# Kernel optimization log

Hardware: AMD Instinct MI355X
Metric: run time of the kernel (lower is better)

The kernel has to match this reference:

```python
import jax, jax.numpy as jnp
import numpy as np

# Model/config constants
N = 2048          # total nodes in batch
G = 32            # number of graphs
NPG = 64          # nodes per graph (N = G * NPG)
E = 16384         # total edges (E//G per graph, unique within graph)
HIDDEN = 256
N_HEADS = 8
HEAD_DIM = HIDDEN // N_HEADS
EDGE_FEAT = 16
SCALE = HEAD_DIM ** -0.5


def setup_inputs() -> dict:
    key = jax.random.key(0)
    ks = jax.random.split(key, 16)
    nodes = jax.random.normal(ks[0], (N, HIDDEN), dtype=jnp.float32)
    edges = jax.random.normal(ks[1], (E, EDGE_FEAT), dtype=jnp.float32)
    n_node = jnp.full((G,), NPG, dtype=jnp.int32)
    # Unique (sender, receiver) pairs within each graph block
    epg = E // G
    gkeys = jax.random.split(ks[2], G)
    perm = jax.vmap(lambda k: jax.random.permutation(k, NPG * NPG)[:epg])(gkeys)  # [G, epg]
    so = perm // NPG
    ro = perm % NPG
    base = (jnp.arange(G, dtype=jnp.int32) * NPG)[:, None]
    senders = (base + so).reshape(-1).astype(jnp.int32)
    receivers = (base + ro).reshape(-1).astype(jnp.int32)
    init = 0.02
    Wq = jax.random.normal(ks[3], (HIDDEN, HIDDEN), jnp.float32) * init
    Wk = jax.random.normal(ks[4], (HIDDEN, HIDDEN), jnp.float32) * init
    Wv = jax.random.normal(ks[5], (HIDDEN, HIDDEN), jnp.float32) * init
    Wo = jax.random.normal(ks[6], (HIDDEN, HIDDEN), jnp.float32) * init
    We = jax.random.normal(ks[7], (EDGE_FEAT, N_HEADS), jnp.float32) * init
    bq = jnp.zeros((HIDDEN,), jnp.float32)
    bk = jnp.zeros((HIDDEN,), jnp.float32)
    bv = jnp.zeros((HIDDEN,), jnp.float32)
    bo = jnp.zeros((HIDDEN,), jnp.float32)
    be = jnp.zeros((N_HEADS,), jnp.float32)
    return {"nodes": nodes, "edges": edges, "n_node": n_node,
            "senders": senders, "receivers": receivers,
            "Wq": Wq, "bq": bq, "Wk": Wk, "bk": bk, "Wv": Wv, "bv": bv,
            "Wo": Wo, "bo": bo, "We": We, "be": be}


def reference(nodes, edges, n_node, senders, receivers,
              Wq, bq, Wk, bk, Wv, bv, Wo, bo, We, be):
    n_nodes = nodes.shape[0]
    n_graphs = n_node.shape[0]
    q = (nodes @ Wq + bq).reshape(n_nodes, N_HEADS, HEAD_DIM)
    k = (nodes @ Wk + bk).reshape(n_nodes, N_HEADS, HEAD_DIM)
    v = (nodes @ Wv + bv).reshape(n_nodes, N_HEADS, HEAD_DIM)
    scores = jnp.einsum('ihd,jhd->ijh', q, k) * SCALE  # [N, N, H]
    graph_idx = jnp.repeat(jnp.arange(n_graphs), n_node, total_repeat_length=n_nodes)
    same_graph = graph_idx[:, None] == graph_idx[None, :]
    scores = scores + jnp.where(same_graph[:, :, None], 0.0, -1e9)
    # Edge bias scattered into [N, N, H] at (receiver, sender)
    edge_bias = edges @ We + be  # [E, H]
    edge_bias_matrix = jnp.zeros((n_nodes, n_nodes, N_HEADS), dtype=scores.dtype)
    edge_bias_matrix = edge_bias_matrix.at[receivers, senders].set(edge_bias)
    scores = scores + edge_bias_matrix
    attn = jax.nn.softmax(scores, axis=1)  # softmax over key axis j
    out = jnp.einsum('ijh,jhd->ihd', attn, v).reshape(n_nodes, HIDDEN)
    return out @ Wo + bo
```

## Files before the change

### kernel.cpp

```cpp
#include <hip/hip_runtime.h>

#define N_NODES 2048
#define N_GRAPHS 32
#define NPG 64
#define N_EDGES 16384
#define EPG 512
#define HIDDEN 256
#define NHEADS 8
#define HEADDIM 32
#define EDGEFEAT 16
#define ATT_SCALE 0.17677669529663687f

typedef unsigned short u16;
typedef __attribute__((ext_vector_type(8))) short bf16x8;
typedef __attribute__((ext_vector_type(4))) float f32x4;

__device__ __forceinline__ u16 f2b(float f) {
    unsigned x = __float_as_uint(f);
    return (u16)((x + 0x7fffu + ((x >> 16) & 1u)) >> 16);
}
__device__ __forceinline__ float b2f(u16 u) {
    return __uint_as_float(((unsigned)u) << 16);
}
__device__ __forceinline__ unsigned pack2(float a, float b) {
    return (unsigned)f2b(a) | ((unsigned)f2b(b) << 16);
}

__global__ __launch_bounds__(256)
void setup_pre(const float* __restrict__ nodes,
               const float* __restrict__ Wq, const float* __restrict__ Wk,
               const float* __restrict__ Wv, const float* __restrict__ Wo,
               const float* __restrict__ edges, const float* __restrict__ We,
               const float* __restrict__ be,
               const int* __restrict__ senders, const int* __restrict__ receivers,
               u16* __restrict__ nodesb,
               u16* __restrict__ WT,
               uint2* __restrict__ ebp,
               float* __restrict__ out)
{
    const int b = blockIdx.x, tid = threadIdx.x;
    __shared__ float sf[64 * 65];

    if (b < 64) {
        const int m = b >> 4, tile = b & 15;
        const int k0 = (tile >> 2) * 64, n0 = (tile & 3) * 64;
        const float* src = (m == 0) ? Wq : (m == 1) ? Wk : (m == 2) ? Wv : Wo;
        u16* dst = WT + m * 65536;
        #pragma unroll
        for (int i = 0; i < 4; ++i) {
            const int idx = i * 256 + tid, kr = idx >> 4, c4 = idx & 15;
            float4 x = *(const float4*)(src + (size_t)(k0 + kr) * HIDDEN + n0 + c4 * 4);
            sf[kr * 65 + c4 * 4 + 0] = x.x;
            sf[kr * 65 + c4 * 4 + 1] = x.y;
            sf[kr * 65 + c4 * 4 + 2] = x.z;
            sf[kr * 65 + c4 * 4 + 3] = x.w;
        }
        __syncthreads();
        #pragma unroll
        for (int i = 0; i < 4; ++i) {
            const int idx = i * 256 + tid, nr = idx >> 4, c4 = idx & 15;
            uint2 w;
            w.x = pack2(sf[(c4 * 4 + 0) * 65 + nr], sf[(c4 * 4 + 1) * 65 + nr]);
            w.y = pack2(sf[(c4 * 4 + 2) * 65 + nr], sf[(c4 * 4 + 3) * 65 + nr]);
            *(uint2*)&dst[(size_t)(n0 + nr) * HIDDEN + k0 + c4 * 4] = w;
        }
    } else if (b < 96) {
        float* sWe = sf;
        float* sbe = sf + 128;
        if (tid < 128) sWe[tid] = We[tid];
        if (tid < 8)  sbe[tid] = be[tid];
        __syncthreads();
        #pragma unroll
        for (int it = 0; it < 2; ++it) {
            const int e = (b - 64) * EPG + it * 256 + tid;
            const float* ep = edges + (size_t)e * EDGEFEAT;
            float4 f0 = *(const float4*)(ep + 0);
            float4 f1 = *(const float4*)(ep + 4);
            float4 f2 = *(const float4*)(ep + 8);
            float4 f3 = *(const float4*)(ep + 12);
            const float ef[16] = {f0.x, f0.y, f0.z, f0.w, f1.x, f1.y, f1.z, f1.w,
                                  f2.x, f2.y, f2.z, f2.w, f3.x, f3.y, f3.z, f3.w};
            const unsigned idx =
                (unsigned)((receivers[e] & (NPG - 1)) * 65 + (senders[e] & (NPG - 1)));
            #pragma unroll
            for (int h = 0; h < NHEADS; ++h) {
                float bias = sbe[h];
                #pragma unroll
                for (int f = 0; f < EDGEFEAT; ++f) bias += ef[f] * sWe[f * 8 + h];
                ebp[(size_t)h * N_EDGES + e] = make_uint2(__float_as_uint(bias), idx);
            }
        }
    } else if (b < 128) {
        const int blk = b - 96;
        #pragma unroll
        for (int it = 0; it < 16; ++it) {
            const int i = blk * 4096 + it * 256 + tid;
            float4 x = ((const float4*)nodes)[i];
            ((uint2*)nodesb)[i] = make_uint2(pack2(x.x, x.y), pack2(x.z, x.w));
        }
    } else {
        const int blk = b - 128;
        const float4 z = make_float4(0.f, 0.f, 0.f, 0.f);
        #pragma unroll
        for (int it = 0; it < 16; ++it)
            ((float4*)out)[blk * 4096 + it * 256 + tid] = z;
    }
}

__global__ __launch_bounds__(256)
void attn_all(const u16* __restrict__ nodesb,
              const u16* __restrict__ WT,
              const float* __restrict__ bq, const float* __restrict__ bk,
              const float* __restrict__ bv, const float* __restrict__ bo,
              const uint2* __restrict__ ebp,
              float* __restrict__ out)
{
    const int g = blockIdx.x, h = blockIdx.y;
    const int tid = threadIdx.x;
    const int lane = tid & 63, wvi = tid >> 6;
    const int l16 = lane & 15, quad = lane >> 4;

    __shared__ __align__(16) unsigned char smem[43776];
    short* qhi = (short*)smem;
    short* qlo = qhi + 2560;
    short* khi = qlo + 2560;
    short* klo = khi + 2560;
    short* vsT = klo + 2560;
    float* sc  = (float*)(smem + 25088);
    float* red = sc + 64 * 65;

    const uint2 e0 = ebp[(size_t)h * N_EDGES + g * EPG + tid];
    const uint2 e1 = ebp[(size_t)h * N_EDGES + g * EPG + 256 + tid];
    float biasv[6];
    #pragma unroll
    for (int nt = 0; nt < 6; ++nt) {
        const int tns = nt >> 1;
        const float* bp = (tns == 0) ? bq : (tns == 1) ? bk : bv;
        biasv[nt] = bp[h * HEADDIM + (nt & 1) * 16 + l16];
    }

    f32x4 acc[6];
    #pragma unroll
    for (int nt = 0; nt < 6; ++nt) acc[nt] = (f32x4){0.f, 0.f, 0.f, 0.f};
    const u16* An = nodesb + (size_t)(g * NPG + wvi * 16 + l16) * HIDDEN + quad * 8;
    #pragma unroll
    for (int k0 = 0; k0 < HIDDEN; k0 += 32) {
        bf16x8 af = *(const bf16x8*)(An + k0);
        #pragma unroll
        for (int nt = 0; nt < 6; ++nt) {
            const u16* bp = WT + (nt >> 1) * 65536
                          + (size_t)(h * HEADDIM + (nt & 1) * 16 + l16) * HIDDEN
                          + k0 + quad * 8;
            acc[nt] = __builtin_amdgcn_mfma_f32_16x16x32_bf16(
                af, *(const bf16x8*)bp, acc[nt], 0, 0, 0);
        }
    }

    #pragma unroll
    for (int nt = 0; nt < 6; ++nt) {
        const int tns = nt >> 1;
        const int col = (nt & 1) * 16 + l16;
        #pragma unroll
        for (int r = 0; r < 4; ++r) {
            const int row = wvi * 16 + quad * 4 + r;
            const float val = acc[nt][r] + biasv[nt];
            if (tns == 2) {
                vsT[col * 72 + row] = (short)f2b(val);
            } else {
                const u16 hi = f2b(val);
                const u16 lo = f2b(val - b2f(hi));
                if (tns == 0) { qhi[row * 40 + col] = (short)hi; qlo[row * 40 + col] = (short)lo; }
                else          { khi[row * 40 + col] = (short)hi; klo[row * 40 + col] = (short)lo; }
            }
        }
    }
    __syncthreads();

    {
        bf16x8 qh = *(const bf16x8*)&qhi[(wvi * 16 + l16) * 40 + quad * 8];
        bf16x8 ql = *(const bf16x8*)&qlo[(wvi * 16 + l16) * 40 + quad * 8];
        #pragma unroll
        for (int nt = 0; nt < 4; ++nt) {
            bf16x8 kh = *(const bf16x8*)&khi[(nt * 16 + l16) * 40 + quad * 8];
            bf16x8 kl = *(const bf16x8*)&klo[(nt * 16 + l16) * 40 + quad * 8];
            f32x4 s = (f32x4){0.f, 0.f, 0.f, 0.f};
            s = __builtin_amdgcn_mfma_f32_16x16x32_bf16(qh, kh, s, 0, 0, 0);
            s = __builtin_amdgcn_mfma_f32_16x16x32_bf16(qh, kl, s, 0, 0, 0);
            s = __builtin_amdgcn_mfma_f32_16x16x32_bf16(ql, kh, s, 0, 0, 0);
            #pragma unroll
            for (int r = 0; r < 4; ++r)
                sc[(wvi * 16 + quad * 4 + r) * 65 + nt * 16 + l16] = s[r] * ATT_SCALE;
        }
    }
    __syncthreads();

    sc[e0.y] += __uint_as_float(e0.x);
    sc[e1.y] += __uint_as_float(e1.x);
    __syncthreads();

    {
        const int i  = tid & 63;
        const int cg = tid >> 6;
        float* red_m = red;
        float* red_s = red + 4 * 64;
        float m = -1e30f;
        #pragma unroll
        for (int jj = 0; jj < 16; ++jj) m = fmaxf(m, sc[i * 65 + cg * 16 + jj]);
        red_m[cg * 64 + i] = m;
        __syncthreads();
        m = fmaxf(fmaxf(red_m[0 * 64 + i], red_m[1 * 64 + i]),
                  fmaxf(red_m[2 * 64 + i], red_m[3 * 64 + i]));
        float s = 0.f;
        #pragma unroll
        for (int jj = 0; jj < 16; ++jj) {
            const int j = cg * 16 + jj;
            float e = __expf(sc[i * 65 + j] - m);
            sc[i * 65 + j] = e;
            s += e;
        }
        red_s[cg * 64 + i] = s;
        __syncthreads();
        const float inv = 1.f / (red_s[0 * 64 + i] + red_s[1 * 64 + i] +
                                 red_s[2 * 64 + i] + red_s[3 * 64 + i]);
        #pragma unroll
        for (int jj = 0; jj < 16; ++jj) sc[i * 65 + cg * 16 + jj] *= inv;
    }
    __syncthreads();

    {
        f32x4 oacc[2];
        oacc[0] = (f32x4){0.f, 0.f, 0.f, 0.f};
        oacc[1] = (f32x4){0.f, 0.f, 0.f, 0.f};
        #pragma unroll
        for (int k0 = 0; k0 < NPG; k0 += 32) {
            float p[8];
            #pragma unroll
            for (int jj = 0; jj < 8; ++jj)
                p[jj] = sc[(wvi * 16 + l16) * 65 + k0 + quad * 8 + jj];
            uint4 uh, ul;
            u16 h0 = f2b(p[0]), h1 = f2b(p[1]), h2 = f2b(p[2]), h3 = f2b(p[3]);
            u16 h4 = f2b(p[4]), h5 = f2b(p[5]), h6 = f2b(p[6]), h7 = f2b(p[7]);
            uh.x = (unsigned)h0 | ((unsigned)h1 << 16);
            uh.y = (unsigned)h2 | ((unsigned)h3 << 16);
            uh.z = (unsigned)h4 | ((unsigned)h5 << 16);
            uh.w = (unsigned)h6 | ((unsigned)h7 << 16);
            ul.x = pack2(p[0] - b2f(h0), p[1] - b2f(h1));
            ul.y = pack2(p[2] - b2f(h2), p[3] - b2f(h3));
            ul.z = pack2(p[4] - b2f(h4), p[5] - b2f(h5));
            ul.w = pack2(p[6] - b2f(h6), p[7] - b2f(h7));
            bf16x8 ph = *(bf16x8*)&uh;
            bf16x8 pl = *(bf16x8*)&ul;
            #pragma unroll
            for (int nt = 0; nt < 2; ++nt) {
                bf16x8 vf = *(const bf16x8*)&vsT[(nt * 16 + l16) * 72 + k0 + quad * 8];
                oacc[nt] = __builtin_amdgcn_mfma_f32_16x16x32_bf16(ph, vf, oacc[nt], 0, 0, 0);
                oacc[nt] = __builtin_amdgcn_mfma_f32_16x16x32_bf16(pl, vf, oacc[nt], 0, 0, 0);
            }
        }
        #pragma unroll
        for (int nt = 0; nt < 2; ++nt) {
            #pragma unroll
            for (int r = 0; r < 4; ++r) {
                const int row = wvi * 16 + quad * 4 + r;
                qhi[row * 40 + nt * 16 + l16] = (short)f2b(oacc[nt][r]);
            }
        }
    }
    __syncthreads();

    {
        bf16x8 afo = *(const bf16x8*)&qhi[(wvi * 16 + l16) * 40 + quad * 8];
        const u16* WoT = WT + 3 * 65536;
        #pragma unroll
        for (int nt = 0; nt < 16; ++nt) {
            const u16* bp = WoT + (size_t)(nt * 16 + l16) * HIDDEN + h * HEADDIM + quad * 8;
            f32x4 c = __builtin_amdgcn_mfma_f32_16x16x32_bf16(
                afo, *(const bf16x8*)bp, (f32x4){0.f, 0.f, 0.f, 0.f}, 0, 0, 0);
            const float bn = (h == 0) ? bo[nt * 16 + l16] : 0.f;
            #pragma unroll
            for (int r = 0; r < 4; ++r)
                atomicAdd(out + (size_t)(g * NPG + wvi * 16 + quad * 4 + r) * HIDDEN
                              + nt * 16 + l16,
                          c[r] + bn);
        }
    }
}

extern "C" void kernel_launch(void* const* d_in, const int* in_sizes, int n_in,
                              void* d_out, int out_size, void* d_ws, size_t ws_size,
                              hipStream_t stream)
{
    const float* nodes     = (const float*)d_in[0];
    const float* edges     = (const float*)d_in[1];
    const int*   senders   = (const int*)d_in[3];
    const int*   receivers = (const int*)d_in[4];
    const float* Wq = (const float*)d_in[5];
    const float* bq = (const float*)d_in[6];
    const float* Wk = (const float*)d_in[7];
    const float* bk = (const float*)d_in[8];
    const float* Wv = (const float*)d_in[9];
    const float* bv = (const float*)d_in[10];
    const float* Wo = (const float*)d_in[11];
    const float* bo = (const float*)d_in[12];
    const float* We = (const float*)d_in[13];
    const float* be = (const float*)d_in[14];
    float* out = (float*)d_out;

    u16*   nodesb = (u16*)d_ws;
    u16*   WT     = (u16*)((char*)d_ws + 1048576);
    uint2* ebp    = (uint2*)((char*)d_ws + 1572864);

    setup_pre<<<dim3(160), dim3(256), 0, stream>>>(
        nodes, Wq, Wk, Wv, Wo, edges, We, be, senders, receivers,
        nodesb, WT, ebp, out);
    attn_all<<<dim3(N_GRAPHS, NHEADS), dim3(256), 0, stream>>>(
        nodesb, WT, bq, bk, bv, bo, ebp, out);
}
```

Before: 113.1 us.

## Split output projection into separate GEMM kernel, drop atomics and bf16 node copy

The output projection no longer runs as per-head atomicAdd accumulation inside the attention kernel. The attention kernel now writes per-head bf16 outputs to a workspace buffer, and a new outproj kernel runs a plain GEMM with bias. Nodes are converted to bf16 on the fly inside the attention kernel, which removes the separate conversion pass and the zeroing of the output in setup. This trades float atomic traffic and setup work for an extra kernel launch and a round trip through global memory for the attention output.

```diff
diff --git a/kernel.cpp b/kernel.cpp
--- a/kernel.cpp
+++ b/kernel.cpp
@@ -27,16 +27,13 @@
 }
 
 __global__ __launch_bounds__(256)
-void setup_pre(const float* __restrict__ nodes,
-               const float* __restrict__ Wq, const float* __restrict__ Wk,
+void setup_pre(const float* __restrict__ Wq, const float* __restrict__ Wk,
                const float* __restrict__ Wv, const float* __restrict__ Wo,
                const float* __restrict__ edges, const float* __restrict__ We,
                const float* __restrict__ be,
                const int* __restrict__ senders, const int* __restrict__ receivers,
-               u16* __restrict__ nodesb,
                u16* __restrict__ WT,
-               uint2* __restrict__ ebp,
-               float* __restrict__ out)
+               uint2* __restrict__ ebp)
 {
     const int b = blockIdx.x, tid = threadIdx.x;
     __shared__ float sf[64 * 65];
@@ -64,56 +61,39 @@
             w.y = pack2(sf[(c4 * 4 + 2) * 65 + nr], sf[(c4 * 4 + 3) * 65 + nr]);
             *(uint2*)&dst[(size_t)(n0 + nr) * HIDDEN + k0 + c4 * 4] = w;
         }
-    } else if (b < 96) {
+    } else {
         float* sWe = sf;
         float* sbe = sf + 128;
         if (tid < 128) sWe[tid] = We[tid];
         if (tid < 8)  sbe[tid] = be[tid];
         __syncthreads();
-        #pragma unroll
-        for (int it = 0; it < 2; ++it) {
-            const int e = (b - 64) * EPG + it * 256 + tid;
-            const float* ep = edges + (size_t)e * EDGEFEAT;
-            float4 f0 = *(const float4*)(ep + 0);
-            float4 f1 = *(const float4*)(ep + 4);
-            float4 f2 = *(const float4*)(ep + 8);
-            float4 f3 = *(const float4*)(ep + 12);
-            const float ef[16] = {f0.x, f0.y, f0.z, f0.w, f1.x, f1.y, f1.z, f1.w,
-                                  f2.x, f2.y, f2.z, f2.w, f3.x, f3.y, f3.z, f3.w};
-            const unsigned idx =
-                (unsigned)((receivers[e] & (NPG - 1)) * 65 + (senders[e] & (NPG - 1)));
-            #pragma unroll
-            for (int h = 0; h < NHEADS; ++h) {
-                float bias = sbe[h];
-                #pragma unroll
-                for (int f = 0; f < EDGEFEAT; ++f) bias += ef[f] * sWe[f * 8 + h];
-                ebp[(size_t)h * N_EDGES + e] = make_uint2(__float_as_uint(bias), idx);
-            }
-        }
-    } else if (b < 128) {
-        const int blk = b - 96;
-        #pragma unroll
-        for (int it = 0; it < 16; ++it) {
-            const int i = blk * 4096 + it * 256 + tid;
-            float4 x = ((const float4*)nodes)[i];
-            ((uint2*)nodesb)[i] = make_uint2(pack2(x.x, x.y), pack2(x.z, x.w));
-        }
-    } else {
-        const int blk = b - 128;
-        const float4 z = make_float4(0.f, 0.f, 0.f, 0.f);
-        #pragma unroll
-        for (int it = 0; it < 16; ++it)
-            ((float4*)out)[blk * 4096 + it * 256 + tid] = z;
+        const int e = (b - 64) * 256 + tid;
+        const float* ep = edges + (size_t)e * EDGEFEAT;
+        float4 f0 = *(const float4*)(ep + 0);
+        float4 f1 = *(const float4*)(ep + 4);
+        float4 f2 = *(const float4*)(ep + 8);
+        float4 f3 = *(const float4*)(ep + 12);
+        const float ef[16] = {f0.x, f0.y, f0.z, f0.w, f1.x, f1.y, f1.z, f1.w,
+                              f2.x, f2.y, f2.z, f2.w, f3.x, f3.y, f3.z, f3.w};
+        const unsigned idx =
+            (unsigned)((receivers[e] & (NPG - 1)) * 65 + (senders[e] & (NPG - 1)));
+        #pragma unroll
+        for (int h = 0; h < NHEADS; ++h) {
+            float bias = sbe[h];
+            #pragma unroll
+            for (int f = 0; f < EDGEFEAT; ++f) bias += ef[f] * sWe[f * 8 + h];
+            ebp[(size_t)h * N_EDGES + e] = make_uint2(__float_as_uint(bias), idx);
+        }
     }
 }
 
 __global__ __launch_bounds__(256)
-void attn_all(const u16* __restrict__ nodesb,
-              const u16* __restrict__ WT,
-              const float* __restrict__ bq, const float* __restrict__ bk,
-              const float* __restrict__ bv, const float* __restrict__ bo,
-              const uint2* __restrict__ ebp,
-              float* __restrict__ out)
+void attn_fused(const float* __restrict__ nodes,
+                const u16* __restrict__ WT,
+                const float* __restrict__ bq, const float* __restrict__ bk,
+                const float* __restrict__ bv,
+                const uint2* __restrict__ ebp,
+                u16* __restrict__ attnb)
 {
     const int g = blockIdx.x, h = blockIdx.y;
     const int tid = threadIdx.x;
@@ -142,10 +122,17 @@
     f32x4 acc[6];
     #pragma unroll
     for (int nt = 0; nt < 6; ++nt) acc[nt] = (f32x4){0.f, 0.f, 0.f, 0.f};
-    const u16* An = nodesb + (size_t)(g * NPG + wvi * 16 + l16) * HIDDEN + quad * 8;
+    const float* Arow = nodes + (size_t)(g * NPG + wvi * 16 + l16) * HIDDEN + quad * 8;
     #pragma unroll
     for (int k0 = 0; k0 < HIDDEN; k0 += 32) {
-        bf16x8 af = *(const bf16x8*)(An + k0);
+        float4 xa = *(const float4*)(Arow + k0);
+        float4 xb = *(const float4*)(Arow + k0 + 4);
+        uint4 ua;
+        ua.x = pack2(xa.x, xa.y);
+        ua.y = pack2(xa.z, xa.w);
+        ua.z = pack2(xb.x, xb.y);
+        ua.w = pack2(xb.z, xb.w);
+        bf16x8 af = *(bf16x8*)&ua;
         #pragma unroll
         for (int nt = 0; nt < 6; ++nt) {
             const u16* bp = WT + (nt >> 1) * 65536
@@ -259,30 +246,49 @@
         }
         #pragma unroll
         for (int nt = 0; nt < 2; ++nt) {
+            const int d = nt * 16 + l16;
             #pragma unroll
             for (int r = 0; r < 4; ++r) {
                 const int row = wvi * 16 + quad * 4 + r;
-                qhi[row * 40 + nt * 16 + l16] = (short)f2b(oacc[nt][r]);
+                attnb[(size_t)(g * NPG + row) * HIDDEN + h * HEADDIM + d] =
+                    f2b(oacc[nt][r]);
             }
         }
     }
-    __syncthreads();
-
-    {
-        bf16x8 afo = *(const bf16x8*)&qhi[(wvi * 16 + l16) * 40 + quad * 8];
-        const u16* WoT = WT + 3 * 65536;
-        #pragma unroll
-        for (int nt = 0; nt < 16; ++nt) {
-            const u16* bp = WoT + (size_t)(nt * 16 + l16) * HIDDEN + h * HEADDIM + quad * 8;
-            f32x4 c = __builtin_amdgcn_mfma_f32_16x16x32_bf16(
-                afo, *(const bf16x8*)bp, (f32x4){0.f, 0.f, 0.f, 0.f}, 0, 0, 0);
-            const float bn = (h == 0) ? bo[nt * 16 + l16] : 0.f;
-            #pragma unroll
-            for (int r = 0; r < 4; ++r)
-                atomicAdd(out + (size_t)(g * NPG + wvi * 16 + quad * 4 + r) * HIDDEN
-                              + nt * 16 + l16,
-                          c[r] + bn);
-        }
+}
+
+__global__ __launch_bounds__(256)
+void outproj(const u16* __restrict__ A,
+             const u16* __restrict__ WoT,
+             const float* __restrict__ bo,
+             float* __restrict__ C)
+{
+    const int n0 = blockIdx.x * 32, m0 = blockIdx.y * 64;
+    const int tid = threadIdx.x;
+    const int lane = tid & 63, wvi = tid >> 6;
+    const int l16 = lane & 15, quad = lane >> 4;
+
+    f32x4 acc[2];
+    acc[0] = (f32x4){0.f, 0.f, 0.f, 0.f};
+    acc[1] = (f32x4){0.f, 0.f, 0.f, 0.f};
+    const u16* Ar = A + (size_t)(m0 + wvi * 16 + l16) * HIDDEN + quad * 8;
+    #pragma unroll
+    for (int k0 = 0; k0 < HIDDEN; k0 += 32) {
+        bf16x8 af = *(const bf16x8*)(Ar + k0);
+        #pragma unroll
+        for (int nt = 0; nt < 2; ++nt) {
+            const u16* bp = WoT + (size_t)(n0 + nt * 16 + l16) * HIDDEN + k0 + quad * 8;
+            acc[nt] = __builtin_amdgcn_mfma_f32_16x16x32_bf16(
+                af, *(const bf16x8*)bp, acc[nt], 0, 0, 0);
+        }
+    }
+    #pragma unroll
+    for (int nt = 0; nt < 2; ++nt) {
+        const int col = n0 + nt * 16 + l16;
+        const float bias = bo[col];
+        #pragma unroll
+        for (int r = 0; r < 4; ++r)
+            C[(size_t)(m0 + wvi * 16 + quad * 4 + r) * HIDDEN + col] = acc[nt][r] + bias;
     }
 }
 
@@ -306,13 +312,14 @@
     const float* be = (const float*)d_in[14];
     float* out = (float*)d_out;
 
-    u16*   nodesb = (u16*)d_ws;
-    u16*   WT     = (u16*)((char*)d_ws + 1048576);
-    uint2* ebp    = (uint2*)((char*)d_ws + 1572864);
-
-    setup_pre<<<dim3(160), dim3(256), 0, stream>>>(
-        nodes, Wq, Wk, Wv, Wo, edges, We, be, senders, receivers,
-        nodesb, WT, ebp, out);
-    attn_all<<<dim3(N_GRAPHS, NHEADS), dim3(256), 0, stream>>>(
-        nodesb, WT, bq, bk, bv, bo, ebp, out);
-}
+    u16*   WT     = (u16*)d_ws;
+    uint2* ebp    = (uint2*)((char*)d_ws + 524288);
+    u16*   attnb  = (u16*)((char*)d_ws + 1572864);
+
+    setup_pre<<<dim3(128), dim3(256), 0, stream>>>(
+        Wq, Wk, Wv, Wo, edges, We, be, senders, receivers, WT, ebp);
+    attn_fused<<<dim3(N_GRAPHS, NHEADS), dim3(256), 0, stream>>>(
+        nodes, WT, bq, bk, bv, ebp, attnb);
+    outproj<<<dim3(HIDDEN / 32, N_NODES / 64), dim3(256), 0, stream>>>(
+        attnb, WT + 3 * 65536, bo, out);
+}
```

Measured after the change: 99.91 us. -11.7%, faster.

## Replace per-head atomic output projection with last-block full Wo GEMM per graph

Applied to the files above, without the earlier changes.

Each head block now writes its bf16 attention output to a global buffer and bumps a per-graph counter. The last head block to finish for a graph runs the full 64x256x256 output projection and stores the result with plain writes, replacing 8-way fp32 atomicAdds into out. This also removes the zero-fill of the output from the setup kernel, and the edge-bias work is spread over more blocks. The cost is serialized tail work on one block per graph plus extra global traffic and fences.

```diff
diff --git a/kernel.cpp b/kernel.cpp
--- a/kernel.cpp
+++ b/kernel.cpp
@@ -27,16 +27,16 @@
 }
 
 __global__ __launch_bounds__(256)
-void setup_pre(const float* __restrict__ nodes,
-               const float* __restrict__ Wq, const float* __restrict__ Wk,
+void setup_pre(const float* __restrict__ Wq, const float* __restrict__ Wk,
                const float* __restrict__ Wv, const float* __restrict__ Wo,
+               const float* __restrict__ nodes,
                const float* __restrict__ edges, const float* __restrict__ We,
                const float* __restrict__ be,
                const int* __restrict__ senders, const int* __restrict__ receivers,
-               u16* __restrict__ nodesb,
                u16* __restrict__ WT,
                uint2* __restrict__ ebp,
-               float* __restrict__ out)
+               u16* __restrict__ nodesb,
+               unsigned* __restrict__ cnt)
 {
     const int b = blockIdx.x, tid = threadIdx.x;
     __shared__ float sf[64 * 65];
@@ -59,61 +59,55 @@
         #pragma unroll
         for (int i = 0; i < 4; ++i) {
             const int idx = i * 256 + tid, nr = idx >> 4, c4 = idx & 15;
-            uint2 w;
-            w.x = pack2(sf[(c4 * 4 + 0) * 65 + nr], sf[(c4 * 4 + 1) * 65 + nr]);
-            w.y = pack2(sf[(c4 * 4 + 2) * 65 + nr], sf[(c4 * 4 + 3) * 65 + nr]);
-            *(uint2*)&dst[(size_t)(n0 + nr) * HIDDEN + k0 + c4 * 4] = w;
-        }
-    } else if (b < 96) {
+            uint2 w2;
+            w2.x = pack2(sf[(c4 * 4 + 0) * 65 + nr], sf[(c4 * 4 + 1) * 65 + nr]);
+            w2.y = pack2(sf[(c4 * 4 + 2) * 65 + nr], sf[(c4 * 4 + 3) * 65 + nr]);
+            *(uint2*)&dst[(size_t)(n0 + nr) * HIDDEN + k0 + c4 * 4] = w2;
+        }
+    } else if (b < 128) {
         float* sWe = sf;
         float* sbe = sf + 128;
         if (tid < 128) sWe[tid] = We[tid];
         if (tid < 8)  sbe[tid] = be[tid];
         __syncthreads();
-        #pragma unroll
-        for (int it = 0; it < 2; ++it) {
-            const int e = (b - 64) * EPG + it * 256 + tid;
-            const float* ep = edges + (size_t)e * EDGEFEAT;
-            float4 f0 = *(const float4*)(ep + 0);
-            float4 f1 = *(const float4*)(ep + 4);
-            float4 f2 = *(const float4*)(ep + 8);
-            float4 f3 = *(const float4*)(ep + 12);
-            const float ef[16] = {f0.x, f0.y, f0.z, f0.w, f1.x, f1.y, f1.z, f1.w,
-                                  f2.x, f2.y, f2.z, f2.w, f3.x, f3.y, f3.z, f3.w};
-            const unsigned idx =
-                (unsigned)((receivers[e] & (NPG - 1)) * 65 + (senders[e] & (NPG - 1)));
-            #pragma unroll
-            for (int h = 0; h < NHEADS; ++h) {
-                float bias = sbe[h];
-                #pragma unroll
-                for (int f = 0; f < EDGEFEAT; ++f) bias += ef[f] * sWe[f * 8 + h];
-                ebp[(size_t)h * N_EDGES + e] = make_uint2(__float_as_uint(bias), idx);
-            }
-        }
-    } else if (b < 128) {
-        const int blk = b - 96;
+        const int e = (b - 64) * 256 + tid;
+        const float* ep = edges + (size_t)e * EDGEFEAT;
+        float4 f0 = *(const float4*)(ep + 0);
+        float4 f1 = *(const float4*)(ep + 4);
+        float4 f2 = *(const float4*)(ep + 8);
+        float4 f3 = *(const float4*)(ep + 12);
+        const float ef[16] = {f0.x, f0.y, f0.z, f0.w, f1.x, f1.y, f1.z, f1.w,
+                              f2.x, f2.y, f2.z, f2.w, f3.x, f3.y, f3.z, f3.w};
+        const unsigned idx =
+            (unsigned)((receivers[e] & (NPG - 1)) * 65 + (senders[e] & (NPG - 1)));
+        #pragma unroll
+        for (int h = 0; h < NHEADS; ++h) {
+            float bias = sbe[h];
+            #pragma unroll
+            for (int f = 0; f < EDGEFEAT; ++f) bias += ef[f] * sWe[f * 8 + h];
+            ebp[(size_t)h * N_EDGES + e] = make_uint2(__float_as_uint(bias), idx);
+        }
+    } else {
+        const int blk = b - 128;
+        if (tid == 0) cnt[blk] = 0u;
         #pragma unroll
         for (int it = 0; it < 16; ++it) {
             const int i = blk * 4096 + it * 256 + tid;
             float4 x = ((const float4*)nodes)[i];
             ((uint2*)nodesb)[i] = make_uint2(pack2(x.x, x.y), pack2(x.z, x.w));
         }
-    } else {
-        const int blk = b - 128;
-        const float4 z = make_float4(0.f, 0.f, 0.f, 0.f);
-        #pragma unroll
-        for (int it = 0; it < 16; ++it)
-            ((float4*)out)[blk * 4096 + it * 256 + tid] = z;
     }
 }
 
 __global__ __launch_bounds__(256)
-void attn_all(const u16* __restrict__ nodesb,
-              const u16* __restrict__ WT,
-              const float* __restrict__ bq, const float* __restrict__ bk,
-              const float* __restrict__ bv, const float* __restrict__ bo,
-              const uint2* __restrict__ ebp,
-              float* __restrict__ out)
+void attn_fused(const u16* __restrict__ nodesb,
+                const u16* __restrict__ WT,
+                const float* __restrict__ bq, const float* __restrict__ bk,
+                const float* __restrict__ bv, const float* __restrict__ bo,
+                const uint2* __restrict__ ebp,
+                u16* __restrict__ attnb,
+                unsigned* __restrict__ cnt,
+                float* __restrict__ out)
 {
     const int g = blockIdx.x, h = blockIdx.y;
     const int tid = threadIdx.x;
@@ -128,6 +122,7 @@
     short* vsT = klo + 2560;
     float* sc  = (float*)(smem + 25088);
     float* red = sc + 64 * 65;
+    __shared__ unsigned slast;
 
     const uint2 e0 = ebp[(size_t)h * N_EDGES + g * EPG + tid];
     const uint2 e1 = ebp[(size_t)h * N_EDGES + g * EPG + 256 + tid];
@@ -259,29 +254,45 @@
         }
         #pragma unroll
         for (int nt = 0; nt < 2; ++nt) {
+            const int d = nt * 16 + l16;
             #pragma unroll
             for (int r = 0; r < 4; ++r) {
                 const int row = wvi * 16 + quad * 4 + r;
-                qhi[row * 40 + nt * 16 + l16] = (short)f2b(oacc[nt][r]);
+                attnb[(size_t)(g * NPG + row) * HIDDEN + h * HEADDIM + d] =
+                    f2b(oacc[nt][r]);
             }
         }
     }
-    __syncthreads();
-
-    {
-        bf16x8 afo = *(const bf16x8*)&qhi[(wvi * 16 + l16) * 40 + quad * 8];
+
+    __threadfence();
+    __syncthreads();
+    if (tid == 0) slast = atomicAdd(&cnt[g], 1u);
+    __syncthreads();
+    if (slast == NHEADS - 1) {
+        __threadfence();
         const u16* WoT = WT + 3 * 65536;
+        f32x4 oc[16];
+        #pragma unroll
+        for (int nt = 0; nt < 16; ++nt) oc[nt] = (f32x4){0.f, 0.f, 0.f, 0.f};
+        const u16* Ar = attnb + (size_t)(g * NPG + wvi * 16 + l16) * HIDDEN + quad * 8;
+        #pragma unroll
+        for (int k0 = 0; k0 < HIDDEN; k0 += 32) {
+            bf16x8 af = *(const bf16x8*)(Ar + k0);
+            #pragma unroll
+            for (int nt = 0; nt < 16; ++nt) {
+                const u16* bp = WoT + (size_t)(nt * 16 + l16) * HIDDEN + k0 + quad * 8;
+                oc[nt] = __builtin_amdgcn_mfma_f32_16x16x32_bf16(
+                    af, *(const bf16x8*)bp, oc[nt], 0, 0, 0);
+            }
+        }
         #pragma unroll
         for (int nt = 0; nt < 16; ++nt) {
-            const u16* bp = WoT + (size_t)(nt * 16 + l16) * HIDDEN + h * HEADDIM + quad * 8;
-            f32x4 c = __builtin_amdgcn_mfma_f32_16x16x32_bf16(
-                afo, *(const bf16x8*)bp, (f32x4){0.f, 0.f, 0.f, 0.f}, 0, 0, 0);
-            const float bn = (h == 0) ? bo[nt * 16 + l16] : 0.f;
+            const int col = nt * 16 + l16;
+            const float bias = bo[col];
             #pragma unroll
             for (int r = 0; r < 4; ++r)
-                atomicAdd(out + (size_t)(g * NPG + wvi * 16 + quad * 4 + r) * HIDDEN
-                              + nt * 16 + l16,
-                          c[r] + bn);
+                out[(size_t)(g * NPG + wvi * 16 + quad * 4 + r) * HIDDEN + col] =
+                    oc[nt][r] + bias;
         }
     }
 }
@@ -306,13 +317,15 @@
     const float* be = (const float*)d_in[14];
     float* out = (float*)d_out;
 
-    u16*   nodesb = (u16*)d_ws;
-    u16*   WT     = (u16*)((char*)d_ws + 1048576);
-    uint2* ebp    = (uint2*)((char*)d_ws + 1572864);
+    u16*      WT     = (u16*)d_ws;
+    uint2*    ebp    = (uint2*)((char*)d_ws + 524288);
+    u16*      nodesb = (u16*)((char*)d_ws + 1572864);
+    u16*      attnb  = (u16*)((char*)d_ws + 2621440);
+    unsigned* cnt    = (unsigned*)((char*)d_ws + 3670016);
 
     setup_pre<<<dim3(160), dim3(256), 0, stream>>>(
-        nodes, Wq, Wk, Wv, Wo, edges, We, be, senders, receivers,
-        nodesb, WT, ebp, out);
-    attn_all<<<dim3(N_GRAPHS, NHEADS), dim3(256), 0, stream>>>(
-        nodesb, WT, bq, bk, bv, bo, ebp, out);
-}
+        Wq, Wk, Wv, Wo, nodes, edges, We, be, senders, receivers,
+        WT, ebp, nodesb, cnt);
+    attn_fused<<<dim3(N_GRAPHS, NHEADS), dim3(256), 0, stream>>>(
+        nodesb, WT, bq, bk, bv, bo, ebp, attnb, cnt, out);
+}
```

New measurement: 148.6 us. +31.3%, slower.
